# Kernel tuning notes

Hardware: AMD Instinct MI355X
Metric: run time of the kernel (lower is better)

Reference implementation:

```python
import jax, jax.numpy as jnp
import numpy as np
import math

B, C, H, W = 8, 384, 14, 14
HEADS = 12
HC = C // HEADS
STRIDE = 2
K = 3
FACTOR = 2.0
rH = -(-H // STRIDE)
rW = -(-W // STRIDE)
N = H * W
S = rH * rW
KK = K * K
OFFSET_MAT = np.array([[0, -1], [-1, -1], [-1, 0], [-1, 1], [0, 1], [1, 1], [1, 0], [1, -1], [0, 0]], dtype=np.float32)


def bilinear_sample(img, coords):
    """img (Hi,Wi,C); coords (...,2) normalized (y,x) in [-1,1].
    Matches F.grid_sample(mode='bilinear', align_corners=True, padding_mode='zeros')."""
    Hi, Wi = img.shape[0], img.shape[1]
    py = (coords[..., 0] + 1.0) * 0.5 * (Hi - 1)
    px = (coords[..., 1] + 1.0) * 0.5 * (Wi - 1)
    y0 = jnp.floor(py)
    x0 = jnp.floor(px)
    wy1 = py - y0
    wx1 = px - x0

    def corner(yf, xf, wgt):
        valid = (yf >= 0) & (yf <= Hi - 1) & (xf >= 0) & (xf <= Wi - 1)
        yi = jnp.clip(yf, 0, Hi - 1).astype(jnp.int32)
        xi = jnp.clip(xf, 0, Wi - 1).astype(jnp.int32)
        return img[yi, xi] * (wgt * valid)[..., None]

    return (corner(y0, x0, (1 - wy1) * (1 - wx1)) + corner(y0, x0 + 1, (1 - wy1) * wx1)
            + corner(y0 + 1, x0, wy1 * (1 - wx1)) + corner(y0 + 1, x0 + 1, wy1 * wx1))


def _forward(x, Wq, bq, Wk, bk, Wv, bv, Wo1, bo1, Wdw, bdw, ln_g, ln_b, Wo2, Wco, posembed, Wp, bp):
    dt = x.dtype
    xh = jnp.transpose(x, (0, 2, 3, 1))                       # B,H,W,C
    q = jnp.einsum('bhwc,oc->bhwo', xh, Wq) + bq              # q_conv (1x1)

    # ---- offset network: 1x1 conv -> GELU -> 3x3 dw stride conv -> LN -> GELU -> 1x1 ----
    t = jax.nn.gelu(jnp.einsum('bhwc,oc->bhwo', q, Wo1) + bo1, approximate=False)
    ker = jnp.transpose(Wdw, (2, 3, 1, 0))                    # (3,3,1,C) for HWIO depthwise
    t = jax.lax.conv_general_dilated(t, ker, (STRIDE, STRIDE), ((1, 1), (1, 1)),
                                     dimension_numbers=('NHWC', 'HWIO', 'NHWC'),
                                     feature_group_count=C) + bdw  # B,rH,rW,C
    mu = t.mean(-1, keepdims=True)
    var = ((t - mu) ** 2).mean(-1, keepdims=True)
    t = (t - mu) / jnp.sqrt(var + 1e-5) * ln_g + ln_b
    t = jax.nn.gelu(t, approximate=False)
    off = jnp.einsum('bhwc,oc->bhwo', t, Wo2)                 # B,rH,rW,2*N ; channel = (g,h,w)
    off = off.reshape(B, rH, rW, 2, N)
    off = jnp.transpose(off, (0, 3, 4, 1, 2))                 # B,2,N,rH,rW
    ranges = jnp.array([1.0 / H, 1.0 / W], dtype=dt)
    off = jnp.tanh(off) * ranges[None, :, None, None, None] * FACTOR
    off = jnp.transpose(off, (0, 2, 3, 4, 1))                 # B,N,rH,rW,2 (y,x)

    # ---- strided reference grid + deformable bilinear gather from x ----
    gy = jnp.arange(0, H, STRIDE, dtype=dt) / (H - 1) * 2 - 1
    gx = jnp.arange(0, W, STRIDE, dtype=dt) / (W - 1) * 2 - 1
    ref = jnp.stack(jnp.meshgrid(gy, gx, indexing='ij'), -1)  # rH,rW,2
    dpos = off + ref
    sampled = jax.vmap(bilinear_sample)(xh, dpos).reshape(B, N, S, C)

    # ---- k x k center points with learned offsets ----
    cy = jnp.arange(H, dtype=dt)
    cx = jnp.arange(W, dtype=dt)
    center = jnp.stack(jnp.meshgrid(cy, cx, indexing='ij'), -1).reshape(N, 1, 2)
    offmat = jnp.asarray(OFFSET_MAT, dtype=dt)
    cpt = center + offmat[None]                               # N,KK,2
    cpt_norm = jnp.stack([jnp.clip(cpt[..., 0], 0, H) / (H - 1) * 2 - 1,
                          jnp.clip(cpt[..., 1], 0, W) / (W - 1) * 2 - 1], -1).reshape(N, K, K, 2)
    q_tok = q.reshape(B, N, C)
    co = jnp.tanh(jnp.einsum('bnc,oc->bno', q_tok, Wco).reshape(B, N, K, K, 2)) * ranges
    cgrid = co + cpt_norm[None]
    csampled = jax.vmap(bilinear_sample)(xh, cgrid).reshape(B, N, KK, C)

    feats = jnp.concatenate([sampled, csampled], axis=2)      # B,N,S+KK,C
    k = (jnp.einsum('bnsc,oc->bnso', feats, Wk) + bk).reshape(B, N, S + KK, HEADS, HC)
    v = (jnp.einsum('bnsc,oc->bnso', feats, Wv) + bv).reshape(B, N, S + KK, HEADS, HC)
    qh = q_tok.reshape(B, N, HEADS, HC)
    attn = jnp.einsum('bnhd,bnshd->bhns', qh, k)              # qk_scale=None -> no scaling

    # ---- dynamic relative position bias (grid_sample into rel-pos table) ----
    a = jnp.arange(0, H, STRIDE, dtype=dt)
    bcol = jnp.arange(0, W, dtype=dt)
    ref_pos = a[None, :] - bcol[:, None]                      # (W, rH)
    ref_pos_x = jnp.tile(ref_pos, (H, rH))                    # (N, S)
    ref_pos_y = jnp.repeat(jnp.repeat(ref_pos, W, axis=0), rW, axis=1)
    rpp = jnp.stack([ref_pos_y / (H - 1), ref_pos_x / (W - 1)], -1)  # N,S,2
    rel = rpp.reshape(N, rH, rW, 2)[None] - off               # B,N,rH,rW,2
    table = jnp.transpose(posembed, (1, 2, 0))                # (2H-1, 2W-1, heads)
    d_rel = bilinear_sample(table, rel).reshape(B, N, S, HEADS)
    cpt_raw = jnp.broadcast_to(center, (N, KK, 2)).reshape(N, K, K, 2)
    crel = co - cpt_raw[None]
    d_crel = bilinear_sample(table, crel).reshape(B, N, KK, HEADS)
    bias = jnp.concatenate([d_rel, d_crel], axis=2)           # B,N,S+KK,heads
    attn = attn + jnp.transpose(bias, (0, 3, 1, 2))
    attn = jax.nn.softmax(attn, axis=-1)

    out = jnp.einsum('bhns,bnshd->bnhd', attn, v).reshape(B, N, C)
    out = jnp.einsum('bnc,oc->bno', out, Wp) + bp             # proj (1x1)
    return jnp.transpose(out.reshape(B, H, W, C), (0, 3, 1, 2))


def setup_inputs() -> dict:
    key = jax.random.key(0)
    ks = jax.random.split(key, 20)
    def w(k, shape, s=0.05):
        return jax.random.normal(k, shape, dtype=jnp.float32) * s
    return {
        'x': jax.random.normal(ks[0], (B, C, H, W), dtype=jnp.float32),
        'Wq': w(ks[1], (C, C)), 'bq': w(ks[2], (C,)),
        'Wk': w(ks[3], (C, C)), 'bk': w(ks[4], (C,)),
        'Wv': w(ks[5], (C, C)), 'bv': w(ks[6], (C,)),
        'Wo1': w(ks[7], (C, C)), 'bo1': w(ks[8], (C,)),
        'Wdw': w(ks[9], (C, 1, 3, 3), 0.2), 'bdw': w(ks[10], (C,)),
        'ln_g': jnp.ones((C,), jnp.float32), 'ln_b': jnp.zeros((C,), jnp.float32),
        'Wo2': w(ks[11], (2 * N, C)),
        'Wco': w(ks[12], (2 * K * K, C)),
        'posembed': w(ks[13], (HEADS, 2 * H - 1, 2 * W - 1), 0.02),
        'Wp': w(ks[14], (C, C)), 'bp': w(ks[15], (C,)),
    }


def reference(x, Wq, bq, Wk, bk, Wv, bv, Wo1, bo1, Wdw, bdw, ln_g, ln_b, Wo2, Wco, posembed, Wp, bp):
    return _forward(x, Wq, bq, Wk, bk, Wv, bv, Wo1, bo1, Wdw, bdw, ln_g, ln_b, Wo2, Wco, posembed, Wp, bp)
```

## Files before the change

### kernel.cpp

```cpp
#include <hip/hip_runtime.h>
#include <hip/hip_bf16.h>
#include <math.h>

#define BB 8
#define CC 384
#define HH 14
#define WW 14
#define NHEADS 12
#define RH 7
#define RW 7
#define NN 196
#define SS 49
#define KKK 9
#define SK 58
#define TH 27
#define NTOK 1568

typedef float    f4 __attribute__((ext_vector_type(4)));
typedef _Float16 h8 __attribute__((ext_vector_type(8)));
typedef _Float16 h4 __attribute__((ext_vector_type(4)));

__device__ __forceinline__ float geluf(float x){ return 0.5f*x*(1.0f+erff(x*0.7071067811865475f)); }
__device__ __forceinline__ f4 mfma16h(h8 a, h8 b, f4 c){
  return __builtin_amdgcn_mfma_f32_16x16x32_f16(a, b, c, 0, 0, 0);
}

__constant__ float c_offm[9][2] = {{0,-1},{-1,-1},{-1,0},{-1,1},{0,1},{1,1},{1,0},{1,-1},{0,0}};

__global__ void __launch_bounds__(256) k_transpose2(const float* __restrict__ x,
                                                    float* __restrict__ xh, _Float16* __restrict__ xhh){
  __shared__ float tile[48*203];
  int b = blockIdx.x >> 3, c0 = (blockIdx.x & 7)*48;
  int t = threadIdx.x;
  for (int i = t; i < 48*49; i += 256){
    int row = i / 49, seg = i % 49;
    f4 v = *(const f4*)(x + ((size_t)(b*CC + c0 + row))*NN + seg*4);
    #pragma unroll
    for (int j = 0; j < 4; ++j) tile[row*203 + seg*4 + j] = v[j];
  }
  __syncthreads();
  for (int i = t; i < 196*12; i += 256){
    int n = i / 12, seg = i % 12;
    f4 v; h4 vh;
    #pragma unroll
    for (int j = 0; j < 4; ++j){ v[j] = tile[(seg*4 + j)*203 + n]; vh[j] = (_Float16)v[j]; }
    size_t o = ((size_t)(b*NN + n))*CC + c0 + seg*4;
    *(f4*)(xh + o) = v;
    *(h4*)(xhh + o) = vh;
  }
}

__device__ __forceinline__ void gemm_hilo_body(
    const float* __restrict__ A, const float* __restrict__ W,
    int arow, int brow, _Float16* sbuf, int t, f4 acc[4]){
  _Float16* Ah = sbuf; _Float16* Al = sbuf + 2560;
  _Float16* Bh = sbuf + 5120; _Float16* Bl = sbuf + 7680;
  int w = t>>6, lane = t&63, col = lane&15, quad = lane>>4;
  int r = t>>2, cg = t&3;
  const float* Ar = A + (size_t)arow*384 + cg*8;
  const float* Br = W + (size_t)brow*384 + cg*8;
  f4 a0 = *(const f4*)(Ar),     a1 = *(const f4*)(Ar + 4);
  f4 b0 = *(const f4*)(Br),     b1 = *(const f4*)(Br + 4);
  for (int k0 = 0; k0 < 384; k0 += 32){
    h8 ah, al, bh, bl;
    #pragma unroll
    for (int j = 0; j < 4; ++j){
      ah[j] = (_Float16)a0[j];   al[j] = (_Float16)(a0[j] - (float)ah[j]);
      ah[4+j] = (_Float16)a1[j]; al[4+j] = (_Float16)(a1[j] - (float)ah[4+j]);
      bh[j] = (_Float16)b0[j];   bl[j] = (_Float16)(b0[j] - (float)bh[j]);
      bh[4+j] = (_Float16)b1[j]; bl[4+j] = (_Float16)(b1[j] - (float)bh[4+j]);
    }
    __syncthreads();
    *(h8*)(Ah + r*40 + cg*8) = ah; *(h8*)(Al + r*40 + cg*8) = al;
    *(h8*)(Bh + r*40 + cg*8) = bh; *(h8*)(Bl + r*40 + cg*8) = bl;
    __syncthreads();
    if (k0 < 352){
      a0 = *(const f4*)(Ar + k0 + 32); a1 = *(const f4*)(Ar + k0 + 36);
      b0 = *(const f4*)(Br + k0 + 32); b1 = *(const f4*)(Br + k0 + 36);
    }
    h8 afh = *(const h8*)(Ah + (w*16+col)*40 + quad*8);
    h8 afl = *(const h8*)(Al + (w*16+col)*40 + quad*8);
    #pragma unroll
    for (int nt = 0; nt < 4; ++nt){
      h8 bfh = *(const h8*)(Bh + (nt*16+col)*40 + quad*8);
      h8 bfl = *(const h8*)(Bl + (nt*16+col)*40 + quad*8);
      acc[nt] = mfma16h(afh, bfh, acc[nt]);
      acc[nt] = mfma16h(afl, bfh, acc[nt]);
      acc[nt] = mfma16h(afh, bfl, acc[nt]);
    }
  }
}

template<int EPI>
__global__ void __launch_bounds__(256) k_mmf(const float* __restrict__ A, const float* __restrict__ W,
                                             const float* __restrict__ bias, float* __restrict__ out,
                                             _Float16* __restrict__ out16, int M, int N){
  __shared__ __align__(16) _Float16 sbuf[10240];
  int t = threadIdx.x;
  int w = t>>6, lane = t&63, col = lane&15, quad = lane>>4;
  int m0 = blockIdx.x*64, n0 = blockIdx.y*64;
  int r = t>>2;
  int arow = min(m0 + r, M-1);
  int brow = min(n0 + r, N-1);
  f4 acc[4] = {{0,0,0,0},{0,0,0,0},{0,0,0,0},{0,0,0,0}};
  gemm_hilo_body(A, W, arow, brow, sbuf, t, acc);
  if constexpr (EPI == 2){
    float* tile = (float*)sbuf;
    __syncthreads();
    #pragma unroll
    for (int nt = 0; nt < 4; ++nt)
      #pragma unroll
      for (int rr = 0; rr < 4; ++rr)
        tile[(w*16 + quad*4 + rr)*65 + nt*16 + col] = acc[nt][rr];
    __syncthreads();
    for (int i = t; i < 1024; i += 256){
      int o_l = i >> 4, ms = i & 15;
      int m = m0 + ms*4;
      if (m >= M) continue;
      int bb = m / NN, nnn = m % NN;
      int o = n0 + o_l;
      float bo = bias[o];
      f4 v = { tile[(ms*4+0)*65 + o_l] + bo, tile[(ms*4+1)*65 + o_l] + bo,
               tile[(ms*4+2)*65 + o_l] + bo, tile[(ms*4+3)*65 + o_l] + bo };
      *(f4*)(out + ((size_t)bb*384 + o)*NN + nnn) = v;
    }
  } else {
    #pragma unroll
    for (int nt = 0; nt < 4; ++nt){
      #pragma unroll
      for (int rr = 0; rr < 4; ++rr){
        int m = m0 + w*16 + quad*4 + rr;
        int o = n0 + nt*16 + col;
        if (m >= M || o >= N) continue;
        float v = acc[nt][rr] + bias[o];
        if (EPI == 1) v = geluf(v);
        out[(size_t)m*384 + o] = v;
      }
    }
  }
}

__global__ void __launch_bounds__(256) k_qkv(
    const float* __restrict__ xh, const _Float16* __restrict__ xhh,
    const float* __restrict__ Wq, const float* __restrict__ bq,
    const float* __restrict__ Wk, const float* __restrict__ Wv,
    float* __restrict__ qf, _Float16* __restrict__ K2h, _Float16* __restrict__ VprojT){
  __shared__ __align__(16) _Float16 sbuf[10240];
  int t = threadIdx.x;
  int w = t>>6, lane = t&63, col = lane&15, quad = lane>>4;
  int bid = blockIdx.x;

  if (bid < 300){
    int isK = (bid >= 150) ? 1 : 0;
    int r2 = isK ? bid - 150 : bid;
    const float* W = isK ? Wk : Wq;
    int m0 = (r2/6)*64, n0 = (r2%6)*64;
    int r = t>>2;
    int arow = min(m0 + r, NTOK-1);
    int brow = n0 + r;
    f4 acc[4] = {{0,0,0,0},{0,0,0,0},{0,0,0,0},{0,0,0,0}};
    gemm_hilo_body(xh, W, arow, brow, sbuf, t, acc);
    #pragma unroll
    for (int nt = 0; nt < 4; ++nt){
      #pragma unroll
      for (int rr = 0; rr < 4; ++rr){
        int m = m0 + w*16 + quad*4 + rr;
        int o = n0 + nt*16 + col;
        if (m >= NTOK) continue;
        if (isK){
          K2h[(size_t)m*384 + o] = (_Float16)acc[nt][rr];
        } else {
          qf[(size_t)m*384 + o] = acc[nt][rr] + bq[o];
        }
      }
    }
  } else {
    int idx = bid - 300;
    int mo = idx % 6;
    int ny = (idx / 6) % 4;
    int b  = idx / 24;
    int m0 = mo*64, n0 = ny*64;
    int orow = m0 + w*16 + col;
    const float* wvr = Wv + (size_t)orow*384;
    f4 acc[4] = {{0,0,0,0},{0,0,0,0},{0,0,0,0},{0,0,0,0}};
    for (int kt = 0; kt < 12; ++kt){
      f4 a0 = *(const f4*)(wvr + kt*32 + quad*8);
      f4 a1 = *(const f4*)(wvr + kt*32 + quad*8 + 4);
      h8 ah, al;
      #pragma unroll
      for (int j = 0; j < 4; ++j){
        ah[j] = (_Float16)a0[j];   al[j] = (_Float16)(a0[j] - (float)ah[j]);
        ah[4+j] = (_Float16)a1[j]; al[4+j] = (_Float16)(a1[j] - (float)ah[4+j]);
      }
      #pragma unroll
      for (int nt = 0; nt < 4; ++nt){
        int i = min(n0 + nt*16 + col, 195);
        h8 b8 = *(const h8*)(xhh + ((size_t)(b*196 + i))*384 + kt*32 + quad*8);
        acc[nt] = mfma16h(ah, b8, acc[nt]);
        acc[nt] = mfma16h(al, b8, acc[nt]);
      }
    }
    #pragma unroll
    for (int nt = 0; nt < 4; ++nt){
      #pragma unroll
      for (int rr = 0; rr < 4; ++rr){
        int o = m0 + w*16 + quad*4 + rr;
        int i = n0 + nt*16 + col;
        if (i < 224)
          VprojT[((size_t)(b*384 + o))*224 + i] = (i < 196) ? (_Float16)acc[nt][rr] : (_Float16)0.f;
      }
    }
  }
}

__global__ void __launch_bounds__(384) k_dwln(const float* __restrict__ t1,
      const float* __restrict__ Wdw, const float* __restrict__ bdw,
      const float* __restrict__ lng, const float* __restrict__ lnb,
      float* __restrict__ t2){
  int blk = blockIdx.x;
  int ow = blk % RW; int oh = (blk / RW) % RH; int b = blk / (RH*RW);
  int c = threadIdx.x;
  float acc = bdw[c];
  #pragma unroll
  for (int kh = 0; kh < 3; ++kh){
    int ih = oh*2 - 1 + kh;
    if (ih < 0 || ih >= HH) continue;
    #pragma unroll
    for (int kw = 0; kw < 3; ++kw){
      int iw = ow*2 - 1 + kw;
      if (iw < 0 || iw >= WW) continue;
      acc += t1[((b*HH + ih)*WW + iw)*CC + c] * Wdw[c*9 + kh*3 + kw];
    }
  }
  __shared__ float red[6];
  __shared__ float s_mu, s_rv;
  float v = acc;
  #pragma unroll
  for (int o = 32; o > 0; o >>= 1) v += __shfl_down(v, o);
  int wid = c >> 6, lane = c & 63;
  if (lane == 0) red[wid] = v;
  __syncthreads();
  if (c == 0){ float s = 0.f; for (int i = 0; i < 6; ++i) s += red[i]; s_mu = s / CC; }
  __syncthreads();
  float mu = s_mu;
  float d = acc - mu;
  v = d*d;
  #pragma unroll
  for (int o = 32; o > 0; o >>= 1) v += __shfl_down(v, o);
  if (lane == 0) red[wid] = v;
  __syncthreads();
  if (c == 0){ float s = 0.f; for (int i = 0; i < 6; ++i) s += red[i]; s_rv = rsqrtf(s / CC + 1e-5f); }
  __syncthreads();
  float val = d * s_rv * lng[c] + lnb[c];
  t2[blk*CC + c] = geluf(val);
}

__global__ void __launch_bounds__(256) k_off(const float* __restrict__ t2, const float* __restrict__ Wo2,
                                             float* __restrict__ offp){
  __shared__ __align__(16) _Float16 sbuf[10240];
  int t = threadIdx.x;
  int w = t>>6, lane = t&63, col = lane&15, quad = lane>>4;
  int bid = blockIdx.x;
  int m0 = (bid/7)*64, n0 = (bid%7)*64;
  int r = t>>2;
  int arow = min(m0 + r, 391);
  int brow = min(n0 + r, 391);
  f4 acc[4] = {{0,0,0,0},{0,0,0,0},{0,0,0,0},{0,0,0,0}};
  gemm_hilo_body(t2, Wo2, arow, brow, sbuf, t, acc);
  #pragma unroll
  for (int nt = 0; nt < 4; ++nt){
    #pragma unroll
    for (int rr = 0; rr < 4; ++rr){
      int row = m0 + w*16 + quad*4 + rr;
      int o = n0 + nt*16 + col;
      if (row < 392 && o < 392){
        int g = o / NN, nn = o % NN;
        int b = row / SS, s = row % SS;
        float rng = (g == 0) ? (1.0f/HH) : (1.0f/WW);
        offp[((b*NN + nn)*SS + s)*2 + g] = tanhf(acc[nt][rr]) * rng * 2.0f;
      }
    }
  }
}

__global__ void __launch_bounds__(256) k_qkt(const float* __restrict__ qf, const _Float16* __restrict__ K2h,
                                             _Float16* __restrict__ G16){
  int t = threadIdx.x;
  int w = t>>6, lane = t&63, col = lane&15, quad = lane>>4;
  int m0 = blockIdx.x*64;
  int bh = blockIdx.y; int b = bh / 12, h = bh - b*12;
  const float* qr = qf + ((size_t)(b*196 + min(m0 + w*16 + col, 195)))*384 + h*32;
  f4 q0 = *(const f4*)(qr + quad*8);
  f4 q1 = *(const f4*)(qr + quad*8 + 4);
  h8 a8;
  #pragma unroll
  for (int j = 0; j < 4; ++j){ a8[j] = (_Float16)q0[j]; a8[4+j] = (_Float16)q1[j]; }
  f4 acc[13];
  #pragma unroll
  for (int nt = 0; nt < 13; ++nt){
    int i = min(nt*16 + col, 195);
    h8 b8 = *(const h8*)(K2h + ((size_t)(b*196 + i))*384 + h*32 + quad*8);
    f4 z = {0.f,0.f,0.f,0.f};
    acc[nt] = mfma16h(a8, b8, z);
  }
  #pragma unroll
  for (int nt = 0; nt < 13; ++nt){
    #pragma unroll
    for (int r = 0; r < 4; ++r){
      int m = m0 + w*16 + quad*4 + r;
      int i = nt*16 + col;
      if (m < 196 && i < 196)
        G16[((size_t)(b*196 + m))*2352 + h*196 + i] = (_Float16)acc[nt][r];
    }
  }
}

__global__ void __launch_bounds__(256, 7) k_fused(
    const float* __restrict__ qf, const float* __restrict__ off,
    const _Float16* __restrict__ G16,
    const float* __restrict__ bk, const float* __restrict__ Wco, const float* __restrict__ pos,
    _Float16* __restrict__ agg16){
  __shared__ __align__(16) _Float16 Gs[2352];
  __shared__ __align__(16) float agg[12*228];
  __shared__ float scoreS[696];
  __shared__ float offl[98];
  __shared__ float colb[18];
  __shared__ float qbv[12];
  __shared__ uint2 tapv[232];
  float* qrow = agg;

  int blk = blockIdx.x;
  int n = blk % NN, b = blk / NN;
  int iy = n / WW, ix = n % WW;
  int t = threadIdx.x;

  {
    const h8* g8 = (const h8*)(G16 + (size_t)blk*2352);
    h8* gs8 = (h8*)Gs;
    for (int i = t; i < 294; i += 256) gs8[i] = g8[i];
  }
  {
    const f4* q4 = (const f4*)(qf + (size_t)blk*384);
    f4* qr4 = (f4*)qrow;
    for (int i = t; i < 96; i += 256) qr4[i] = q4[i];
  }
  for (int i = t; i < 98; i += 256) offl[i] = off[(size_t)blk*98 + i];
  __syncthreads();

  if (t < 144){
    int o = t >> 3, l = t & 7;
    const float* wr = Wco + o*384 + l*48;
    const float* qr = qrow + l*48;
    f4 a4 = {0.f,0.f,0.f,0.f};
    #pragma unroll
    for (int c = 0; c < 48; c += 4) a4 += (*(const f4*)(qr + c)) * (*(const f4*)(wr + c));
    float acc = a4[0]+a4[1]+a4[2]+a4[3];
    acc += __shfl_xor(acc, 1); acc += __shfl_xor(acc, 2); acc += __shfl_xor(acc, 4);
    if (l == 0){
      int g = o & 1;
      float range = (g == 0) ? (1.0f/HH) : (1.0f/WW);
      colb[o] = tanhf(acc) * range;
    }
  }
  if (t >= 160){
    int o = t - 160;
    int h = o >> 3, l = o & 7;
    float acc = 0.f;
    for (int d = l; d < 32; d += 8) acc += qrow[h*32 + d] * bk[h*32 + d];
    acc += __shfl_xor(acc, 1); acc += __shfl_xor(acc, 2); acc += __shfl_xor(acc, 4);
    if (l == 0 && h < 12) qbv[h] = acc;
  }
  __syncthreads();

  if (t < SK){
    float cy, cx;
    if (t < SS){
      int sy = t / RW, sx = t % RW;
      cy = offl[t*2+0] + ((2.0f*sy)/13.0f*2.0f - 1.0f);
      cx = offl[t*2+1] + ((2.0f*sx)/13.0f*2.0f - 1.0f);
    } else {
      int kk = t - SS;
      float cyr = fminf(fmaxf((float)iy + c_offm[kk][0], 0.f), (float)HH);
      float cxr = fminf(fmaxf((float)ix + c_offm[kk][1], 0.f), (float)WW);
      cy = colb[kk*2+0] + (cyr/13.0f*2.0f - 1.0f);
      cx = colb[kk*2+1] + (cxr/13.0f*2.0f - 1.0f);
    }
    float py = (cy + 1.0f)*0.5f*13.0f;
    float px = (cx + 1.0f)*0.5f*13.0f;
    float y0 = floorf(py), x0 = floorf(px);
    float wy1 = py - y0, wx1 = px - x0;
    #pragma unroll
    for (int k4 = 0; k4 < 4; ++k4){
      float yf = y0 + (k4 >> 1), xf = x0 + (k4 & 1);
      bool valid = (yf >= 0.f) && (yf <= 13.f) && (xf >= 0.f) && (xf <= 13.f);
      int yi = (int)fminf(fmaxf(yf, 0.f), 13.f);
      int xi = (int)fminf(fmaxf(xf, 0.f), 13.f);
      float wgt = ((k4 >> 1) ? wy1 : (1.f - wy1)) * ((k4 & 1) ? wx1 : (1.f - wx1));
      tapv[t*4 + k4] = make_uint2(__float_as_uint(valid ? wgt : 0.f),
                                  (unsigned)(yi*WW + xi));
    }
  }
  __syncthreads();
  for (int i = t; i < 12*228; i += 256) agg[i] = 0.f;

  for (int i = t; i < SK*NHEADS; i += 256){
    int s = i / NHEADS, h = i - s*NHEADS;
    float ry, rx;
    if (s < SS){
      int sy = s / RW, sx = s % RW;
      ry = (2.0f*sy - iy)/13.0f - offl[s*2+0];
      rx = (2.0f*sx - ix)/13.0f - offl[s*2+1];
    } else {
      int kk = s - SS;
      ry = colb[kk*2+0] - (float)iy;
      rx = colb[kk*2+1] - (float)ix;
    }
    float py = (ry + 1.0f)*0.5f*26.0f;
    float px = (rx + 1.0f)*0.5f*26.0f;
    float y0 = floorf(py), x0 = floorf(px);
    float wy1 = py - y0, wx1 = px - x0;
    float val = qbv[h];
    #pragma unroll
    for (int k4 = 0; k4 < 4; ++k4){
      float yf = y0 + (k4 >> 1), xf = x0 + (k4 & 1);
      if (yf >= 0.f && yf <= 26.f && xf >= 0.f && xf <= 26.f){
        int yi = (int)yf, xi = (int)xf;
        float wgt = ((k4 >> 1) ? wy1 : (1.f - wy1)) * ((k4 & 1) ? wx1 : (1.f - wx1));
        val += pos[(h*TH + yi)*TH + xi] * wgt;
      }
    }
    #pragma unroll
    for (int k4 = 0; k4 < 4; ++k4){
      uint2 tp = tapv[s*4 + k4];
      val += __uint_as_float(tp.x) * (float)Gs[h*196 + (int)tp.y];
    }
    scoreS[h*58 + s] = val;
  }
  __syncthreads();

  if (t < 192){
    int h = t >> 4, l = t & 15;
    float v[4];
    #pragma unroll
    for (int k = 0; k < 4; ++k){ int s = l + 16*k; v[k] = (s < SK) ? scoreS[h*58 + s] : -1e30f; }
    float mx = fmaxf(fmaxf(v[0], v[1]), fmaxf(v[2], v[3]));
    mx = fmaxf(mx, __shfl_xor(mx, 1)); mx = fmaxf(mx, __shfl_xor(mx, 2));
    mx = fmaxf(mx, __shfl_xor(mx, 4)); mx = fmaxf(mx, __shfl_xor(mx, 8));
    float e[4], sum = 0.f;
    #pragma unroll
    for (int k = 0; k < 4; ++k){ int s = l + 16*k; e[k] = (s < SK) ? expf(v[k] - mx) : 0.f; sum += e[k]; }
    sum += __shfl_xor(sum, 1); sum += __shfl_xor(sum, 2);
    sum += __shfl_xor(sum, 4); sum += __shfl_xor(sum, 8);
    float inv = 1.0f / sum;
    #pragma unroll
    for (int k = 0; k < 4; ++k){
      int s = l + 16*k;
      if (s < SK) scoreS[h*58 + s] = e[k]*inv;
    }
  }
  __syncthreads();

  for (int i = t; i < 232*NHEADS; i += 256){
    int tap = i / NHEADS, h = i - tap*NHEADS;
    int s = tap >> 2;
    uint2 tp = tapv[tap];
    float v = scoreS[h*58 + s] * __uint_as_float(tp.x);
    atomicAdd(&agg[h*228 + (int)tp.y], v);
  }
  __syncthreads();

  {
    _Float16* ar = agg16 + (size_t)blk*2688;
    for (int i = t; i < 336; i += 256){
      int d = i*8;
      int h = d / 224, j = d - h*224;
      const float* src = agg + h*228 + j;
      f4 a = *(const f4*)src;
      f4 c = *(const f4*)(src + 4);
      h8 o;
      #pragma unroll
      for (int k = 0; k < 4; ++k){ o[k] = (_Float16)a[k]; o[4+k] = (_Float16)c[k]; }
      *(h8*)(ar + d) = o;
    }
  }
}

__global__ void __launch_bounds__(256) k_av(const _Float16* __restrict__ agg16,
                                            const _Float16* __restrict__ VprojT,
                                            const float* __restrict__ bv, float* __restrict__ otok){
  int t = threadIdx.x;
  int w = t>>6, lane = t&63, col = lane&15, quad = lane>>4;
  int m0 = blockIdx.x*64;
  int bh = blockIdx.y; int b = bh / 12, h = bh - b*12;
  const _Float16* ar = agg16 + ((size_t)(b*196 + min(m0 + w*16 + col, 195)))*2688 + h*224;
  f4 acc[2] = {{0,0,0,0},{0,0,0,0}};
  for (int kt = 0; kt < 7; ++kt){
    h8 a8 = *(const h8*)(ar + kt*32 + quad*8);
    #pragma unroll
    for (int nt = 0; nt < 2; ++nt){
      int o = h*32 + nt*16 + col;
      h8 b8 = *(const h8*)(VprojT + ((size_t)(b*384 + o))*224 + kt*32 + quad*8);
      acc[nt] = mfma16h(a8, b8, acc[nt]);
    }
  }
  #pragma unroll
  for (int nt = 0; nt < 2; ++nt){
    #pragma unroll
    for (int rr = 0; rr < 4; ++rr){
      int m = m0 + w*16 + quad*4 + rr;
      if (m < 196){
        int o = h*32 + nt*16 + col;
        otok[((size_t)(b*196 + m))*384 + o] = acc[nt][rr] + bv[o];
      }
    }
  }
}

extern "C" void kernel_launch(void* const* d_in, const int* in_sizes, int n_in,
                              void* d_out, int out_size, void* d_ws, size_t ws_size,
                              hipStream_t stream){
  const float* x    = (const float*)d_in[0];
  const float* Wq   = (const float*)d_in[1];
  const float* bq   = (const float*)d_in[2];
  const float* Wk   = (const float*)d_in[3];
  const float* bk   = (const float*)d_in[4];
  const float* Wv   = (const float*)d_in[5];
  const float* bv   = (const float*)d_in[6];
  const float* Wo1  = (const float*)d_in[7];
  const float* bo1  = (const float*)d_in[8];
  const float* Wdw  = (const float*)d_in[9];
  const float* bdw  = (const float*)d_in[10];
  const float* ln_g = (const float*)d_in[11];
  const float* ln_b = (const float*)d_in[12];
  const float* Wo2  = (const float*)d_in[13];
  const float* Wco  = (const float*)d_in[14];
  const float* pos  = (const float*)d_in[15];
  const float* Wp   = (const float*)d_in[16];
  const float* bp   = (const float*)d_in[17];
  float* out = (float*)d_out;

  float* ws   = (float*)d_ws;
  float* xh   = ws;
  float* qf   = xh   + 602112;
  float* t1   = qf   + 602112;
  float* t2   = t1   + 602112;
  float* offp = t2   + 150528;
  float* otok = offp + 153664;
  _Float16* xhh    = (_Float16*)(otok + 602112);
  _Float16* K2h    = xhh    + 602112;
  _Float16* VprojT = K2h    + 602112;
  _Float16* G16    = VprojT + 688128;
  _Float16* agg16  = G16    + 3687936;

  k_transpose2<<<64, 256, 0, stream>>>(x, xh, xhh);
  k_qkv<<<492, 256, 0, stream>>>(xh, xhh, Wq, bq, Wk, Wv, qf, K2h, VprojT);
  k_mmf<1><<<dim3(25,6), 256, 0, stream>>>(qf, Wo1, bo1, t1, nullptr, NTOK, 384);
  k_dwln<<<392, 384, 0, stream>>>(t1, Wdw, bdw, ln_g, ln_b, t2);
  k_off<<<49, 256, 0, stream>>>(t2, Wo2, offp);
  k_qkt<<<dim3(4,96), 256, 0, stream>>>(qf, K2h, G16);
  k_fused<<<1568, 256, 0, stream>>>(qf, offp, G16, bk, Wco, pos, agg16);
  k_av<<<dim3(4,96), 256, 0, stream>>>(agg16, VprojT, bv, otok);
  k_mmf<2><<<dim3(25,6), 256, 0, stream>>>(otok, Wp, bp, out, nullptr, NTOK, 384);
}
```

Measured before the change: 207.8 us.

## Merge Wo1 GEMM and QK^T into one launch; restructure score and scatter loops

The offset-network 1x1 GEMM (Wo1+GELU) and the independent QK^T kernel now run as two block ranges of a single kernel, which removes one launch and lets the two independent jobs overlap on the GPU. In the fused attention kernel, each thread now handles one sample and three heads, so the positional bilinear indices and weights are computed once and shared across those heads instead of once per (sample, head). The scatter step is now one thread per tap looping over all 12 heads, and it skips taps whose weight is zero. In exchange, block work in the merged kernel is uneven and each scatter thread issues more serial atomics.

```diff
diff --git a/kernel.cpp b/kernel.cpp
--- a/kernel.cpp
+++ b/kernel.cpp
@@ -283,34 +283,57 @@
   }
 }
 
-__global__ void __launch_bounds__(256) k_qkt(const float* __restrict__ qf, const _Float16* __restrict__ K2h,
-                                             _Float16* __restrict__ G16){
+__global__ void __launch_bounds__(256) k_mid(const float* __restrict__ qf, const float* __restrict__ Wo1,
+                                             const float* __restrict__ bo1, float* __restrict__ t1,
+                                             const _Float16* __restrict__ K2h, _Float16* __restrict__ G16){
+  __shared__ __align__(16) _Float16 sbuf[10240];
   int t = threadIdx.x;
   int w = t>>6, lane = t&63, col = lane&15, quad = lane>>4;
-  int m0 = blockIdx.x*64;
-  int bh = blockIdx.y; int b = bh / 12, h = bh - b*12;
-  const float* qr = qf + ((size_t)(b*196 + min(m0 + w*16 + col, 195)))*384 + h*32;
-  f4 q0 = *(const f4*)(qr + quad*8);
-  f4 q1 = *(const f4*)(qr + quad*8 + 4);
-  h8 a8;
-  #pragma unroll
-  for (int j = 0; j < 4; ++j){ a8[j] = (_Float16)q0[j]; a8[4+j] = (_Float16)q1[j]; }
-  f4 acc[13];
-  #pragma unroll
-  for (int nt = 0; nt < 13; ++nt){
-    int i = min(nt*16 + col, 195);
-    h8 b8 = *(const h8*)(K2h + ((size_t)(b*196 + i))*384 + h*32 + quad*8);
-    f4 z = {0.f,0.f,0.f,0.f};
-    acc[nt] = mfma16h(a8, b8, z);
-  }
-  #pragma unroll
-  for (int nt = 0; nt < 13; ++nt){
-    #pragma unroll
-    for (int r = 0; r < 4; ++r){
-      int m = m0 + w*16 + quad*4 + r;
-      int i = nt*16 + col;
-      if (m < 196 && i < 196)
-        G16[((size_t)(b*196 + m))*2352 + h*196 + i] = (_Float16)acc[nt][r];
+  int bid = blockIdx.x;
+  if (bid < 150){
+    int m0 = (bid/6)*64, n0 = (bid%6)*64;
+    int r = t>>2;
+    int arow = min(m0 + r, NTOK-1);
+    int brow = n0 + r;
+    f4 acc[4] = {{0,0,0,0},{0,0,0,0},{0,0,0,0},{0,0,0,0}};
+    gemm_hilo_body(qf, Wo1, arow, brow, sbuf, t, acc);
+    #pragma unroll
+    for (int nt = 0; nt < 4; ++nt){
+      #pragma unroll
+      for (int rr = 0; rr < 4; ++rr){
+        int m = m0 + w*16 + quad*4 + rr;
+        int o = n0 + nt*16 + col;
+        if (m >= NTOK) continue;
+        t1[(size_t)m*384 + o] = geluf(acc[nt][rr] + bo1[o]);
+      }
+    }
+  } else {
+    int idx = bid - 150;
+    int m0 = (idx & 3)*64;
+    int bh = idx >> 2; int b = bh / 12, h = bh - b*12;
+    const float* qr = qf + ((size_t)(b*196 + min(m0 + w*16 + col, 195)))*384 + h*32;
+    f4 q0 = *(const f4*)(qr + quad*8);
+    f4 q1 = *(const f4*)(qr + quad*8 + 4);
+    h8 a8;
+    #pragma unroll
+    for (int j = 0; j < 4; ++j){ a8[j] = (_Float16)q0[j]; a8[4+j] = (_Float16)q1[j]; }
+    f4 acc[13];
+    #pragma unroll
+    for (int nt = 0; nt < 13; ++nt){
+      int i = min(nt*16 + col, 195);
+      h8 b8 = *(const h8*)(K2h + ((size_t)(b*196 + i))*384 + h*32 + quad*8);
+      f4 z = {0.f,0.f,0.f,0.f};
+      acc[nt] = mfma16h(a8, b8, z);
+    }
+    #pragma unroll
+    for (int nt = 0; nt < 13; ++nt){
+      #pragma unroll
+      for (int r = 0; r < 4; ++r){
+        int m = m0 + w*16 + quad*4 + r;
+        int i = nt*16 + col;
+        if (m < 196 && i < 196)
+          G16[((size_t)(b*196 + m))*2352 + h*196 + i] = (_Float16)acc[nt][r];
+      }
     }
   }
 }
@@ -403,8 +426,8 @@
   __syncthreads();
   for (int i = t; i < 12*228; i += 256) agg[i] = 0.f;
 
-  for (int i = t; i < SK*NHEADS; i += 256){
-    int s = i / NHEADS, h = i - s*NHEADS;
+  if (t < 232){
+    int s = t >> 2, grp = t & 3;
     float ry, rx;
     if (s < SS){
       int sy = s / RW, sx = s % RW;
@@ -419,22 +442,36 @@
     float px = (rx + 1.0f)*0.5f*26.0f;
     float y0 = floorf(py), x0 = floorf(px);
     float wy1 = py - y0, wx1 = px - x0;
-    float val = qbv[h];
+    int pidx[4]; float pw[4];
     #pragma unroll
     for (int k4 = 0; k4 < 4; ++k4){
       float yf = y0 + (k4 >> 1), xf = x0 + (k4 & 1);
-      if (yf >= 0.f && yf <= 26.f && xf >= 0.f && xf <= 26.f){
-        int yi = (int)yf, xi = (int)xf;
-        float wgt = ((k4 >> 1) ? wy1 : (1.f - wy1)) * ((k4 & 1) ? wx1 : (1.f - wx1));
-        val += pos[(h*TH + yi)*TH + xi] * wgt;
-      }
-    }
-    #pragma unroll
-    for (int k4 = 0; k4 < 4; ++k4){
-      uint2 tp = tapv[s*4 + k4];
-      val += __uint_as_float(tp.x) * (float)Gs[h*196 + (int)tp.y];
-    }
-    scoreS[h*58 + s] = val;
+      bool valid = (yf >= 0.f) && (yf <= 26.f) && (xf >= 0.f) && (xf <= 26.f);
+      int yi = (int)fminf(fmaxf(yf, 0.f), 26.f);
+      int xi = (int)fminf(fmaxf(xf, 0.f), 26.f);
+      pidx[k4] = yi*TH + xi;
+      float wgt = ((k4 >> 1) ? wy1 : (1.f - wy1)) * ((k4 & 1) ? wx1 : (1.f - wx1));
+      pw[k4] = valid ? wgt : 0.f;
+    }
+    uint2 tp0 = tapv[s*4+0], tp1 = tapv[s*4+1], tp2 = tapv[s*4+2], tp3 = tapv[s*4+3];
+    float tw0 = __uint_as_float(tp0.x), tw1 = __uint_as_float(tp1.x);
+    float tw2 = __uint_as_float(tp2.x), tw3 = __uint_as_float(tp3.x);
+    #pragma unroll
+    for (int hh = 0; hh < 3; ++hh){
+      int h = grp*3 + hh;
+      const float* pt = pos + h*729;
+      float val = qbv[h];
+      val += pt[pidx[0]]*pw[0];
+      val += pt[pidx[1]]*pw[1];
+      val += pt[pidx[2]]*pw[2];
+      val += pt[pidx[3]]*pw[3];
+      const _Float16* gh = Gs + h*196;
+      val += tw0*(float)gh[(int)tp0.y];
+      val += tw1*(float)gh[(int)tp1.y];
+      val += tw2*(float)gh[(int)tp2.y];
+      val += tw3*(float)gh[(int)tp3.y];
+      scoreS[h*58 + s] = val;
+    }
   }
   __syncthreads();
 
@@ -460,12 +497,16 @@
   }
   __syncthreads();
 
-  for (int i = t; i < 232*NHEADS; i += 256){
-    int tap = i / NHEADS, h = i - tap*NHEADS;
-    int s = tap >> 2;
-    uint2 tp = tapv[tap];
-    float v = scoreS[h*58 + s] * __uint_as_float(tp.x);
-    atomicAdd(&agg[h*228 + (int)tp.y], v);
+  if (t < 232){
+    uint2 tp = tapv[t];
+    float wv = __uint_as_float(tp.x);
+    if (wv != 0.f){
+      int s = t >> 2, cell = (int)tp.y;
+      float* ag = agg + cell;
+      #pragma unroll
+      for (int h = 0; h < 12; ++h)
+        atomicAdd(ag + h*228, scoreS[h*58 + s]*wv);
+    }
   }
   __syncthreads();
 
@@ -554,10 +595,9 @@
 
   k_transpose2<<<64, 256, 0, stream>>>(x, xh, xhh);
   k_qkv<<<492, 256, 0, stream>>>(xh, xhh, Wq, bq, Wk, Wv, qf, K2h, VprojT);
-  k_mmf<1><<<dim3(25,6), 256, 0, stream>>>(qf, Wo1, bo1, t1, nullptr, NTOK, 384);
+  k_mid<<<534, 256, 0, stream>>>(qf, Wo1, bo1, t1, K2h, G16);
   k_dwln<<<392, 384, 0, stream>>>(t1, Wdw, bdw, ln_g, ln_b, t2);
   k_off<<<49, 256, 0, stream>>>(t2, Wo2, offp);
-  k_qkt<<<dim3(4,96), 256, 0, stream>>>(qf, K2h, G16);
   k_fused<<<1568, 256, 0, stream>>>(qf, offp, G16, bk, Wco, pos, agg16);
   k_av<<<dim3(4,96), 256, 0, stream>>>(agg16, VprojT, bv, otok);
   k_mmf<2><<<dim3(25,6), 256, 0, stream>>>(otok, Wp, bp, out, nullptr, NTOK, 384);
```

Result: faster. 198.3 us (-4.6%).
